# Kernel optimization log

Hardware: AMD Instinct MI355X
Metric: run time of the kernel (lower is better)

Reference implementation:

```python
import jax, jax.numpy as jnp
import numpy as np

INPUT_SIZE = 1024
ATTN_SIZE = 1024


def setup_inputs() -> dict:
    key = jax.random.key(0)
    ks = jax.random.split(key, 7)
    s = 1.0 / np.sqrt(INPUT_SIZE)
    x = jax.random.normal(ks[0], (2048, 8, INPUT_SIZE), dtype=jnp.float32)
    Wq = jax.random.uniform(ks[1], (ATTN_SIZE, INPUT_SIZE), jnp.float32, -s, s)
    bq = jax.random.uniform(ks[2], (ATTN_SIZE,), jnp.float32, -s, s)
    Wk = jax.random.uniform(ks[3], (ATTN_SIZE, INPUT_SIZE), jnp.float32, -s, s)
    bk = jax.random.uniform(ks[4], (ATTN_SIZE,), jnp.float32, -s, s)
    Wv = jax.random.uniform(ks[5], (ATTN_SIZE, INPUT_SIZE), jnp.float32, -s, s)
    bv = jax.random.uniform(ks[6], (ATTN_SIZE,), jnp.float32, -s, s)
    return {"x": x, "Wq": Wq, "bq": bq, "Wk": Wk, "bk": bk, "Wv": Wv, "bv": bv}


def reference(x, Wq, bq, Wk, bk, Wv, bv):
    # x: (S, B, D) -> (B, S, D)
    xb = jnp.swapaxes(x, 0, 1)
    Q = jnp.einsum('bsd,ad->bsa', xb, Wq) + bq  # (B, S, A)
    K = jnp.einsum('bsd,ad->bsa', xb, Wk) + bk
    V = jnp.einsum('bsd,ad->bsa', xb, Wv) + bv
    S = Q.shape[1]
    scores = jnp.einsum('bqa,bka->bqk', Q, K) / jnp.sqrt(jnp.float32(ATTN_SIZE))
    causal = jnp.tril(jnp.ones((S, S), dtype=bool))  # True where attended
    scores = jnp.where(causal, scores, -jnp.inf)
    probs = jax.nn.softmax(scores, axis=-1)
    out = jnp.einsum('bqk,bka->bqa', probs, V)  # (B, S, A)
    return jnp.swapaxes(out, 0, 1)  # (S, B, A)
```

## Files before the change

kernel.cpp:

```cpp
#include <hip/hip_runtime.h>
#include <hip/hip_bf16.h>
#include <math.h>

typedef short bf16x8 __attribute__((ext_vector_type(8)));
typedef float f32x4 __attribute__((ext_vector_type(4)));
typedef short short4v __attribute__((ext_vector_type(4)));
typedef short short8v __attribute__((ext_vector_type(8)));

__device__ __forceinline__ short f2bf(float f) {
  unsigned u = __builtin_bit_cast(unsigned, f);
  unsigned r = (u + 0x7FFFu + ((u >> 16) & 1u)) >> 16;
  return (short)r;
}
__device__ __forceinline__ float bf2f(short s) {
  unsigned u = ((unsigned)(unsigned short)s) << 16;
  return __builtin_bit_cast(float, u);
}

typedef __attribute__((address_space(1))) const unsigned g_u32;
typedef __attribute__((address_space(3))) unsigned l_u32;
__device__ __forceinline__ void gload_lds16(const short* g, short* l) {
  __builtin_amdgcn_global_load_lds((g_u32*)g, (l_u32*)l, 16, 0, 0);
}

#define VMCNT(n) asm volatile("s_waitcnt vmcnt(" #n ")" ::: "memory")

__global__ __launch_bounds__(256) void k_cast(const float* __restrict__ x,
                                              const float* __restrict__ Wq, const float* __restrict__ Wk,
                                              const float* __restrict__ Wv, const float* __restrict__ bq,
                                              const float* __restrict__ bk, const float* __restrict__ bv,
                                              short* __restrict__ xb, short* __restrict__ Wcat,
                                              float* __restrict__ biascat) {
  int bid = blockIdx.x;
  if (bid < 16384) {
    int tid = bid * 256 + threadIdx.x;
    int d4 = tid & 255;
    int sb = tid >> 8;
    int s = sb & 2047;
    int b = sb >> 11;
    float4 v = *((const float4*)(x + (((size_t)s * 8 + b) << 10)) + d4);
    short4v o;
    o.x = f2bf(v.x); o.y = f2bf(v.y); o.z = f2bf(v.z); o.w = f2bf(v.w);
    *((short4v*)(xb + (((size_t)b * 2048 + s) << 10)) + d4) = o;
  } else if (bid < 19456) {
    int tid = (bid - 16384) * 256 + threadIdx.x;
    int d4 = tid & 255;
    int n = tid >> 8;
    const float* src = (n < 1024) ? Wq : (n < 2048 ? Wk : Wv);
    int nl = n & 1023;
    float4 v = *((const float4*)(src + ((size_t)nl << 10)) + d4);
    short4v o;
    o.x = f2bf(v.x); o.y = f2bf(v.y); o.z = f2bf(v.z); o.w = f2bf(v.w);
    *((short4v*)(Wcat + ((size_t)n << 10)) + d4) = o;
  } else {
    int i = (bid - 19456) * 256 + threadIdx.x;
    if (i < 3072) biascat[i] = (i < 1024) ? bq[i] : (i < 2048 ? bk[i & 1023] : bv[i & 1023]);
  }
}

template <int LDA, int LDB>
__device__ __forceinline__ void gemm128n_core(const short* __restrict__ Ag, const short* __restrict__ Bg,
                                              int NC, short* __restrict__ lds, f32x4 (&acc)[4][4], int tid) {
  const int lane = tid & 63;
  const int wid = tid >> 6;
  const int wm = wid >> 1, wn = wid & 1;
  const int r15 = lane & 15;
  const int g = lane >> 4;
  const int co = ((g ^ ((r15 >> 1) & 3)) << 3);
  short* As = lds;
  short* Bs = lds + 3 * 8192;

  const int abase = (wm * 64 + r15) * 32 + co;
  const int bbase = (wn * 64 + r15) * 32 + co;

  auto stage_pair = [&](int c) {
    short* Ap = As + (c % 3) * 8192;
    short* Bp = Bs + (c % 3) * 4096;
    int kb = c << 5;
#pragma unroll
    for (int i = 0; i < 2; ++i) {
      int ch = i * 512 + tid;
      int r = ch >> 2, s = ch & 3;
      gload_lds16(Ag + (size_t)r * LDA + kb + ((s ^ ((r >> 1) & 3)) << 3), Ap + ch * 8);
    }
    {
      int r = tid >> 2, s = tid & 3;
      gload_lds16(Bg + (size_t)r * LDB + kb + ((s ^ ((r >> 1) & 3)) << 3), Bp + tid * 8);
    }
  };

  auto phase = [&](int c, bool stage, bool last) {
    bf16x8 a4[4], br[4];
    const short* pa = As + (c % 3) * 8192 + abase;
    const short* pb = Bs + (c % 3) * 4096 + bbase;
#pragma unroll
    for (int mf = 0; mf < 4; ++mf) a4[mf] = *(const bf16x8*)(pa + mf * 512);
#pragma unroll
    for (int nf = 0; nf < 4; ++nf) br[nf] = *(const bf16x8*)(pb + nf * 512);
    if (stage) {
      stage_pair(c + 2);
      VMCNT(3);
    } else if (!last) {
      VMCNT(0);
    }
    __builtin_amdgcn_s_barrier();
    asm volatile("s_waitcnt lgkmcnt(0)" ::: "memory");
    __builtin_amdgcn_sched_barrier(0);
    __builtin_amdgcn_s_setprio(1);
#pragma unroll
    for (int mf = 0; mf < 4; ++mf)
#pragma unroll
      for (int nf = 0; nf < 4; ++nf)
        acc[mf][nf] = __builtin_amdgcn_mfma_f32_16x16x32_bf16(a4[mf], br[nf], acc[mf][nf], 0, 0, 0);
    __builtin_amdgcn_s_setprio(0);
    __builtin_amdgcn_s_barrier();
  };

  stage_pair(0);
  stage_pair(1);
  VMCNT(3);
  __builtin_amdgcn_s_barrier();

  for (int c = 0; c < NC - 2; ++c) phase(c, true, false);
  phase(NC - 2, false, false);
  phase(NC - 1, false, true);
}

__global__ __launch_bounds__(512, 4) void k_proj(const short* __restrict__ Xb, const short* __restrict__ Wc,
                                                 const float* __restrict__ biascat,
                                                 short* __restrict__ Q, short* __restrict__ K, short* __restrict__ Vt) {
  __shared__ __align__(16) short lds[36864];
  int tid = threadIdx.x;
  int wg = blockIdx.x;
  int swz = (wg & 7) * 192 + (wg >> 3);
  int mt = swz / 24, nt = swz % 24;
  int m0 = mt << 8, n0 = nt << 7;
  f32x4 acc[4][4] = {};
  gemm128n_core<1024, 1024>(Xb + (size_t)m0 * 1024, Wc + (size_t)n0 * 1024, 32, lds, acc, tid);
  int lane = tid & 63, wid = tid >> 6;
  int wm = wid >> 1, wn = wid & 1;
  int r15 = lane & 15, g = lane >> 4;
  int which = n0 >> 10;
  int nbase = n0 & 1023;
  if (which == 2) {
#pragma unroll
    for (int ni = 0; ni < 4; ++ni) {
      int cth = wn * 64 + ni * 16 + r15;
      int a = nbase + cth;
      float bv = biascat[n0 + cth];
#pragma unroll
      for (int mi = 0; mi < 4; ++mi) {
        int r = m0 + wm * 64 + mi * 16 + g * 4;
        int b = r >> 11, s = r & 2047;
        short4v o;
#pragma unroll
        for (int j = 0; j < 4; ++j) o[j] = f2bf(acc[mi][ni][j] + bv);
        *(short4v*)(Vt + ((size_t)b << 21) + ((size_t)a << 11) + s) = o;
      }
    }
  } else {
    short* outb = (which == 0) ? Q : K;
#pragma unroll
    for (int ni = 0; ni < 4; ++ni) {
      int cth = wn * 64 + ni * 16 + r15;
      float bv = biascat[n0 + cth];
#pragma unroll
      for (int mi = 0; mi < 4; ++mi)
#pragma unroll
        for (int j = 0; j < 4; ++j) {
          int r = m0 + wm * 64 + mi * 16 + g * 4 + j;
          outb[((size_t)r << 10) + nbase + cth] = f2bf(acc[mi][ni][j] + bv);
        }
    }
  }
}

__global__ __launch_bounds__(512, 4) void k_qk(const short* __restrict__ Q, const short* __restrict__ K,
                                               short* __restrict__ Sc) {
  __shared__ __align__(16) short lds[36864];
  int f = blockIdx.x;
  int b = f & 7;
  int idx = f >> 3;
  int mt = (int)((sqrtf(4.f * idx + 1.f) - 1.f) * 0.5f);
  while ((mt + 1) * (mt + 2) <= idx) ++mt;
  while (mt * (mt + 1) > idx) --mt;
  int nt = idx - mt * (mt + 1);
  int tid = threadIdx.x;
  int m0 = mt << 8, n0 = nt << 7;
  const short* Qb = Q + ((size_t)b << 21);
  const short* Kb = K + ((size_t)b << 21);
  f32x4 acc[4][4] = {};
  gemm128n_core<1024, 1024>(Qb + (size_t)m0 * 1024, Kb + (size_t)n0 * 1024, 32, lds, acc, tid);
  short* Sb = Sc + ((size_t)b << 22);
  int lane = tid & 63, wid = tid >> 6;
  int wm = wid >> 1, wn = wid & 1;
  int r15 = lane & 15, g = lane >> 4;
#pragma unroll
  for (int mi = 0; mi < 4; ++mi)
#pragma unroll
    for (int ni = 0; ni < 4; ++ni)
#pragma unroll
      for (int j = 0; j < 4; ++j) {
        int r = m0 + wm * 64 + mi * 16 + g * 4 + j;
        int c = n0 + wn * 64 + ni * 16 + r15;
        Sb[((size_t)r << 11) + c] = f2bf(acc[mi][ni][j] * 0.03125f);
      }
}

__global__ __launch_bounds__(256) void k_softmax(short* __restrict__ Sc) {
  int row = blockIdx.x * 4 + (threadIdx.x >> 6);
  int lane = threadIdx.x & 63;
  int b = row >> 11, q = row & 2047;
  short* Pr = Sc + ((size_t)b << 22) + ((size_t)q << 11);
  int T = ((q >> 8) + 1) << 8;
  float v[4][8];
  float mx = -__builtin_inff();
#pragma unroll
  for (int it = 0; it < 4; ++it) {
    int k0 = it * 512 + lane * 8;
    if (k0 < T) {
      short8v raw = *(const short8v*)(Pr + k0);
#pragma unroll
      for (int j = 0; j < 8; ++j) {
        float xv = (k0 + j <= q) ? bf2f(raw[j]) : -__builtin_inff();
        v[it][j] = xv;
        mx = fmaxf(mx, xv);
      }
    }
  }
  for (int off = 1; off < 64; off <<= 1) mx = fmaxf(mx, __shfl_xor(mx, off, 64));
  float sum = 0.f;
#pragma unroll
  for (int it = 0; it < 4; ++it) {
    int k0 = it * 512 + lane * 8;
    if (k0 < T) {
#pragma unroll
      for (int j = 0; j < 8; ++j) {
        float e = exp2f((v[it][j] - mx) * 1.4426950408889634f);
        v[it][j] = e;
        sum += e;
      }
    }
  }
  for (int off = 1; off < 64; off <<= 1) sum += __shfl_xor(sum, off, 64);
  float inv = 1.f / sum;
#pragma unroll
  for (int it = 0; it < 4; ++it) {
    int k0 = it * 512 + lane * 8;
    if (k0 < T) {
      short8v o;
#pragma unroll
      for (int j = 0; j < 8; ++j) o[j] = (k0 + j <= q) ? f2bf(v[it][j] * inv) : (short)0;
      *(short8v*)(Pr + k0) = o;
    }
  }
}

__global__ __launch_bounds__(512, 4) void k_pv(const short* __restrict__ P, const short* __restrict__ Vt,
                                               float* __restrict__ out) {
  __shared__ __align__(16) short lds[36864];
  int f = blockIdx.x;
  int b = f & 7;
  int idx = f >> 3;
  int half = idx >> 5, j = idx & 31;
  int mt = half ? (7 - (j >> 2)) : (j >> 2);
  int nt = half ? (4 + (j & 3)) : (j & 3);
  int tid = threadIdx.x;
  int m0 = mt << 8, n0 = nt << 7;
  int NC = 8 * (mt + 1);
  const short* Pb = P + ((size_t)b << 22);
  const short* Vtb = Vt + ((size_t)b << 21);
  f32x4 acc[4][4] = {};
  gemm128n_core<2048, 2048>(Pb + (size_t)m0 * 2048, Vtb + (size_t)n0 * 2048, NC, lds, acc, tid);
  int lane = tid & 63, wid = tid >> 6;
  int wm = wid >> 1, wn = wid & 1;
  int r15 = lane & 15, g = lane >> 4;
#pragma unroll
  for (int mi = 0; mi < 4; ++mi)
#pragma unroll
    for (int ni = 0; ni < 4; ++ni)
#pragma unroll
      for (int j2 = 0; j2 < 4; ++j2) {
        int r = m0 + wm * 64 + mi * 16 + g * 4 + j2;
        int c = n0 + wn * 64 + ni * 16 + r15;
        out[((size_t)r << 13) + ((size_t)b << 10) + c] = acc[mi][ni][j2];
      }
}

extern "C" void kernel_launch(void* const* d_in, const int* in_sizes, int n_in,
                              void* d_out, int out_size, void* d_ws, size_t ws_size,
                              hipStream_t stream) {
  const float* x  = (const float*)d_in[0];
  const float* Wq = (const float*)d_in[1];
  const float* bq = (const float*)d_in[2];
  const float* Wk = (const float*)d_in[3];
  const float* bk = (const float*)d_in[4];
  const float* Wv = (const float*)d_in[5];
  const float* bv = (const float*)d_in[6];
  float* out = (float*)d_out;
  char* ws = (char*)d_ws;

  short* xb   = (short*)(ws);
  short* Wcat = (short*)(ws + 33554432);
  float* bias = (float*)(ws + 39845888);
  short* Q    = (short*)(ws + 39858176);
  short* K    = (short*)(ws + 73412608);
  short* Vt   = (short*)(ws + 106967040);
  short* Sc   = (short*)(ws + 140521472);

  k_cast<<<19468, 256, 0, stream>>>(x, Wq, Wk, Wv, bq, bk, bv, xb, Wcat, bias);
  k_proj<<<1536, 512, 0, stream>>>(xb, Wcat, bias, Q, K, Vt);
  k_qk<<<576, 512, 0, stream>>>(Q, K, Sc);
  k_softmax<<<4096, 256, 0, stream>>>(Sc);
  k_pv<<<512, 512, 0, stream>>>(Sc, Vt, out);
}
```

Baseline: 261.0 us.

## Double-buffer LDS fragment reads in register ping-pong to overlap with MFMA

The GEMM core now keeps two register sets of A/B fragments, so LDS reads for chunk c+1 are issued before the MFMAs on chunk c. Each step then needs one barrier instead of two, and global prefetch runs three stages ahead. The aim is to hide LDS read latency behind matrix math and cut barrier stalls. In exchange, register use grows, and launch bounds drop from 4 to 2 waves-per-EU minimum to allow more VGPRs, which can lower occupancy. Reusing the 3-slot ring with a lookahead of 3 needs careful barrier ordering to avoid overwriting slots that are still being read.

```diff
diff --git a/kernel.cpp b/kernel.cpp
--- a/kernel.cpp
+++ b/kernel.cpp
@@ -24,6 +24,7 @@
 }
 
 #define VMCNT(n) asm volatile("s_waitcnt vmcnt(" #n ")" ::: "memory")
+#define LGKM(n) asm volatile("s_waitcnt lgkmcnt(" #n ")" ::: "memory")
 
 __global__ __launch_bounds__(256) void k_cast(const float* __restrict__ x,
                                               const float* __restrict__ Wq, const float* __restrict__ Wk,
@@ -59,7 +60,7 @@
 }
 
 template <int LDA, int LDB>
-__device__ __forceinline__ void gemm128n_core(const short* __restrict__ Ag, const short* __restrict__ Bg,
+__device__ __forceinline__ void gemm128p_core(const short* __restrict__ Ag, const short* __restrict__ Bg,
                                               int NC, short* __restrict__ lds, f32x4 (&acc)[4][4], int tid) {
   const int lane = tid & 63;
   const int wid = tid >> 6;
@@ -89,23 +90,16 @@
     }
   };
 
-  auto phase = [&](int c, bool stage, bool last) {
-    bf16x8 a4[4], br[4];
+  bf16x8 aA[4], bA[4], aB[4], bB[4];
+  auto rd = [&](bf16x8 (&a4)[4], bf16x8 (&br)[4], int c) {
     const short* pa = As + (c % 3) * 8192 + abase;
     const short* pb = Bs + (c % 3) * 4096 + bbase;
 #pragma unroll
     for (int mf = 0; mf < 4; ++mf) a4[mf] = *(const bf16x8*)(pa + mf * 512);
 #pragma unroll
     for (int nf = 0; nf < 4; ++nf) br[nf] = *(const bf16x8*)(pb + nf * 512);
-    if (stage) {
-      stage_pair(c + 2);
-      VMCNT(3);
-    } else if (!last) {
-      VMCNT(0);
-    }
-    __builtin_amdgcn_s_barrier();
-    asm volatile("s_waitcnt lgkmcnt(0)" ::: "memory");
-    __builtin_amdgcn_sched_barrier(0);
+  };
+  auto mm = [&](bf16x8 (&a4)[4], bf16x8 (&br)[4]) {
     __builtin_amdgcn_s_setprio(1);
 #pragma unroll
     for (int mf = 0; mf < 4; ++mf)
@@ -113,20 +107,47 @@
       for (int nf = 0; nf < 4; ++nf)
         acc[mf][nf] = __builtin_amdgcn_mfma_f32_16x16x32_bf16(a4[mf], br[nf], acc[mf][nf], 0, 0, 0);
     __builtin_amdgcn_s_setprio(0);
-    __builtin_amdgcn_s_barrier();
+  };
+  auto waits = [&](int c) {
+    if (c + 3 < NC) {
+      stage_pair(c + 3);
+      VMCNT(3);
+    } else if (c + 3 == NC) {
+      VMCNT(0);
+    }
   };
 
   stage_pair(0);
   stage_pair(1);
   VMCNT(3);
   __builtin_amdgcn_s_barrier();
-
-  for (int c = 0; c < NC - 2; ++c) phase(c, true, false);
-  phase(NC - 2, false, false);
-  phase(NC - 1, false, true);
-}
-
-__global__ __launch_bounds__(512, 4) void k_proj(const short* __restrict__ Xb, const short* __restrict__ Wc,
+  rd(aA, bA, 0);
+  stage_pair(2);
+  VMCNT(3);
+  LGKM(0);
+  __builtin_amdgcn_s_barrier();
+
+  int c = 0;
+  for (; c + 3 < NC; c += 2) {
+    rd(aB, bB, c + 1);
+    waits(c);
+    mm(aA, bA);
+    LGKM(0);
+    __builtin_amdgcn_s_barrier();
+    rd(aA, bA, c + 2);
+    waits(c + 1);
+    mm(aB, bB);
+    LGKM(0);
+    __builtin_amdgcn_s_barrier();
+  }
+  rd(aB, bB, NC - 1);
+  mm(aA, bA);
+  LGKM(0);
+  __builtin_amdgcn_s_barrier();
+  mm(aB, bB);
+}
+
+__global__ __launch_bounds__(512, 2) void k_proj(const short* __restrict__ Xb, const short* __restrict__ Wc,
                                                  const float* __restrict__ biascat,
                                                  short* __restrict__ Q, short* __restrict__ K, short* __restrict__ Vt) {
   __shared__ __align__(16) short lds[36864];
@@ -136,7 +157,7 @@
   int mt = swz / 24, nt = swz % 24;
   int m0 = mt << 8, n0 = nt << 7;
   f32x4 acc[4][4] = {};
-  gemm128n_core<1024, 1024>(Xb + (size_t)m0 * 1024, Wc + (size_t)n0 * 1024, 32, lds, acc, tid);
+  gemm128p_core<1024, 1024>(Xb + (size_t)m0 * 1024, Wc + (size_t)n0 * 1024, 32, lds, acc, tid);
   int lane = tid & 63, wid = tid >> 6;
   int wm = wid >> 1, wn = wid & 1;
   int r15 = lane & 15, g = lane >> 4;
@@ -175,7 +196,7 @@
   }
 }
 
-__global__ __launch_bounds__(512, 4) void k_qk(const short* __restrict__ Q, const short* __restrict__ K,
+__global__ __launch_bounds__(512, 2) void k_qk(const short* __restrict__ Q, const short* __restrict__ K,
                                                short* __restrict__ Sc) {
   __shared__ __align__(16) short lds[36864];
   int f = blockIdx.x;
@@ -190,7 +211,7 @@
   const short* Qb = Q + ((size_t)b << 21);
   const short* Kb = K + ((size_t)b << 21);
   f32x4 acc[4][4] = {};
-  gemm128n_core<1024, 1024>(Qb + (size_t)m0 * 1024, Kb + (size_t)n0 * 1024, 32, lds, acc, tid);
+  gemm128p_core<1024, 1024>(Qb + (size_t)m0 * 1024, Kb + (size_t)n0 * 1024, 32, lds, acc, tid);
   short* Sb = Sc + ((size_t)b << 22);
   int lane = tid & 63, wid = tid >> 6;
   int wm = wid >> 1, wn = wid & 1;
@@ -256,7 +277,7 @@
   }
 }
 
-__global__ __launch_bounds__(512, 4) void k_pv(const short* __restrict__ P, const short* __restrict__ Vt,
+__global__ __launch_bounds__(512, 2) void k_pv(const short* __restrict__ P, const short* __restrict__ Vt,
                                                float* __restrict__ out) {
   __shared__ __align__(16) short lds[36864];
   int f = blockIdx.x;
@@ -271,7 +292,7 @@
   const short* Pb = P + ((size_t)b << 22);
   const short* Vtb = Vt + ((size_t)b << 21);
   f32x4 acc[4][4] = {};
-  gemm128n_core<2048, 2048>(Pb + (size_t)m0 * 2048, Vtb + (size_t)n0 * 2048, NC, lds, acc, tid);
+  gemm128p_core<2048, 2048>(Pb + (size_t)m0 * 2048, Vtb + (size_t)n0 * 2048, NC, lds, acc, tid);
   int lane = tid & 63, wid = tid >> 6;
   int wm = wid >> 1, wn = wid & 1;
   int r15 = lane & 15, g = lane >> 4;
```

Result: no change. 265.1 us (+1.6%).
